# Performance work log

Hardware: AMD Instinct MI355X
Metric: run time of the kernel (lower is better)

Reference implementation:

```python
import jax, jax.numpy as jnp
import numpy as np

K_DELTA = 2.0
K_AN = 2.0
N_CLASSES = 32


def _masked_mean(x, mask):
    m = mask.astype(x.dtype)
    return jnp.sum(x * m) / jnp.maximum(jnp.sum(m), 1.0)


def setup_inputs() -> dict:
    key = jax.random.key(0)
    k1, k2 = jax.random.split(key)
    logits = jax.random.normal(k1, (384, 1024), dtype=jnp.float32)
    labels = jax.random.randint(k2, (384,), 0, N_CLASSES)
    return {"logits": logits, "labels": labels}


def reference(logits, labels):
    # Faithful jit-safe translation: torch.where / torch.unique produce
    # dynamic-shaped index lists; here we return the equivalent boolean
    # masks over the full triplet / pair space instead.
    N = labels.shape[0]
    x = jax.lax.stop_gradient(logits)  # logits.detach()
    x = x / jnp.linalg.norm(x, axis=1, keepdims=True)  # F.normalize p=2 dim=1
    mat = -(x @ x.T)  # negative cosine similarity, symmetric [N, N]

    sames = labels[:, None] == labels[None, :]
    diffs = ~sames
    sames = sames & ~jnp.eye(N, dtype=bool)  # fill_diagonal_(0)
    # triplet validity mask over (anchor, positive, negative)
    trip = sames[:, :, None] & diffs[:, None, :]  # [N, N, N]

    # delta[a, p, n] = an_dist - ap_dist
    delta = mat[:, None, :] - mat[:, :, None]  # [N, N, N]

    # --- calc_loss_an branch: unique (anchor, negative) pairs ---
    # a pair (a, n) appears in some triplet iff diffs[a, n] and anchor a has
    # at least one positive; unique_filter canonicalizes to (min, max).
    has_pos = jnp.any(sames, axis=1)  # [N]
    upper = jnp.triu(jnp.ones((N, N), dtype=bool), k=1)
    pair_mask = upper & diffs & (has_pos[:, None] | has_pos[None, :])
    an_mean = _masked_mean(mat, pair_mask)
    beta = 1.0 + (-an_mean - 1.0) / K_AN  # self.update(an_dist_unique, 'an')
    an_pairs = pair_mask & (-mat >= beta)

    # --- epsilon update + semi-hard triplet selection ---
    eps = jnp.clip(_masked_mean(delta, trip) / K_DELTA, 0.0, 0.5)
    cond = trip & (delta <= eps) & (delta > 0.0)  # semi-hard

    return cond, an_pairs, eps, beta
```

## Files before the change

kernel.cpp:

```cpp
#include <hip/hip_runtime.h>
#include <stdint.h>

#define N 384
#define D 1024
#define N2 (N * N)
static constexpr size_t N3 = (size_t)N * N2;

static constexpr size_t PART_OFF = 0;
static constexpr size_t MAT_OFF  = 2359296;
static constexpr size_t INVN_OFF = 3538944;
static constexpr size_t TN_OFF   = 3542016;
static constexpr size_t TC_OFF   = 3545088;
static constexpr size_t ANS_OFF  = 3548160;
static constexpr size_t ANC_OFF  = 3551232;
static constexpr size_t HP_OFF   = 3554304;
static constexpr size_t SC_OFF   = 3555840;

static constexpr int GEMM_BLOCKS = 288;
static constexpr int FILL_BLOCKS = 2048;
static constexpr size_t FILL_F4  = 14192640;

__global__ __launch_bounds__(256) void k_invnorm(const float* __restrict__ x,
                                                 double* __restrict__ invn) {
  int w = threadIdx.x >> 6, lane = threadIdx.x & 63;
  int a = blockIdx.x * 4 + w;
  const float4* row = (const float4*)(x + (size_t)a * D);
  double s = 0.0;
#pragma unroll
  for (int j = 0; j < 4; ++j) {
    float4 v = row[lane + 64 * j];
    double dx = v.x, dy = v.y, dz = v.z, dw = v.w;
    s += dx * dx + dy * dy + dz * dz + dw * dw;
  }
#pragma unroll
  for (int m = 32; m; m >>= 1) s += __shfl_xor(s, m, 64);
  if (lane == 0) invn[a] = 1.0 / sqrt(s);
}

__global__ __launch_bounds__(256) void k_mega(const float* __restrict__ x,
                                              const double* __restrict__ invn,
                                              double* __restrict__ part,
                                              float4* __restrict__ outv) {
  __shared__ double As[64][32];
  __shared__ double Bs[64][32];
  int b = blockIdx.x;
  int t = threadIdx.x;
  if (b >= GEMM_BLOCKS) {
    size_t i = (size_t)(b - GEMM_BLOCKS) * 256 + t;
    const size_t stride = (size_t)FILL_BLOCKS * 256;
    float4 z = make_float4(0.f, 0.f, 0.f, 0.f);
    for (; i < FILL_F4; i += stride) outv[i] = z;
    return;
  }
  int bz = b / 144, rem = b % 144;
  int m0 = (rem % 12) * 32, n0 = (rem / 12) * 32, k0 = bz * 512;
  int tm = t & 15, tn = t >> 4;
  double a00 = 0, a01 = 0, a10 = 0, a11 = 0;
  for (int kc = 0; kc < 8; ++kc) {
    int kbase = k0 + kc * 64;
#pragma unroll
    for (int h = 0; h < 2; ++h) {
      int f = t + h * 256;
      int m = f & 31, kq = f >> 5;
      float4 va = *(const float4*)(x + (size_t)(m0 + m) * D + kbase + kq * 4);
      As[kq * 4 + 0][m] = (double)va.x; As[kq * 4 + 1][m] = (double)va.y;
      As[kq * 4 + 2][m] = (double)va.z; As[kq * 4 + 3][m] = (double)va.w;
      float4 vb = *(const float4*)(x + (size_t)(n0 + m) * D + kbase + kq * 4);
      Bs[kq * 4 + 0][m] = (double)vb.x; Bs[kq * 4 + 1][m] = (double)vb.y;
      Bs[kq * 4 + 2][m] = (double)vb.z; Bs[kq * 4 + 3][m] = (double)vb.w;
    }
    __syncthreads();
#pragma unroll 8
    for (int k = 0; k < 64; ++k) {
      double ax = As[k][2 * tm], ay = As[k][2 * tm + 1];
      double bx = Bs[k][2 * tn], by = Bs[k][2 * tn + 1];
      a00 = fma(ax, bx, a00);
      a01 = fma(ax, by, a01);
      a10 = fma(ay, bx, a10);
      a11 = fma(ay, by, a11);
    }
    __syncthreads();
  }
  int r0 = m0 + 2 * tm, c0 = n0 + 2 * tn;
  double i0 = invn[r0], i1 = invn[r0 + 1], j0 = invn[c0], j1 = invn[c0 + 1];
  double* o = part + (size_t)bz * N2;
  o[(size_t)r0 * N + c0]           = a00 * (i0 * j0);
  o[(size_t)r0 * N + c0 + 1]       = a01 * (i0 * j1);
  o[(size_t)(r0 + 1) * N + c0]     = a10 * (i1 * j0);
  o[(size_t)(r0 + 1) * N + c0 + 1] = a11 * (i1 * j1);
}

__global__ __launch_bounds__(384) void k_stats(const double* __restrict__ part,
                                               const int* __restrict__ labels,
                                               double* __restrict__ mat,
                                               double* __restrict__ tn,
                                               double* __restrict__ tc,
                                               double* __restrict__ ans,
                                               double* __restrict__ anc,
                                               int* __restrict__ hp) {
  __shared__ int labs[N];
  __shared__ int hist[32];
  __shared__ double cw[6][6];
  int a = blockIdx.x, t = threadIdx.x;
  int w = t >> 6, lane = t & 63;
  if (t < 32) hist[t] = 0;
  labs[t] = labels[t];
  __syncthreads();
  atomicAdd(&hist[labs[t] & 31], 1);
  __syncthreads();
  int la = labs[a];
  double m = -(part[(size_t)a * N + t] + part[(size_t)N2 + (size_t)a * N + t]);
  mat[(size_t)a * N + t] = m;
  bool same = (labs[t] == la) && (t != a);
  bool diff = (labs[t] != la);
  bool hpa = hist[la] >= 2;
  bool hpt = hist[labs[t]] >= 2;
  bool anm = (t > a) && diff && (hpa || hpt);

  double q[6];
  q[0] = same ? m : 0.0;
  q[1] = same ? 1.0 : 0.0;
  q[2] = diff ? m : 0.0;
  q[3] = diff ? 1.0 : 0.0;
  q[4] = anm ? m : 0.0;
  q[5] = anm ? 1.0 : 0.0;
#pragma unroll
  for (int i = 0; i < 6; ++i) {
#pragma unroll
    for (int s = 32; s; s >>= 1) q[i] += __shfl_xor(q[i], s, 64);
  }
  if (lane == 0) {
#pragma unroll
    for (int i = 0; i < 6; ++i) cw[w][i] = q[i];
  }
  __syncthreads();
  if (t == 0) {
    double r[6];
#pragma unroll
    for (int i = 0; i < 6; ++i) {
      double s = 0.0;
      for (int ww = 0; ww < 6; ++ww) s += cw[ww][i];
      r[i] = s;
    }
    tn[a]  = r[2] * r[1] - r[0] * r[3];
    tc[a]  = r[1] * r[3];
    ans[a] = r[4];
    anc[a] = r[5];
    hp[a]  = hpa ? 1 : 0;
  }
}

__global__ __launch_bounds__(64) void k_final(const double* __restrict__ tn,
                                              const double* __restrict__ tc,
                                              const double* __restrict__ ans,
                                              const double* __restrict__ anc,
                                              double* __restrict__ sc,
                                              float* __restrict__ out_tail) {
  int t = threadIdx.x;
  double vtn = 0, vtc = 0, vas = 0, vac = 0;
#pragma unroll
  for (int j = 0; j < 6; ++j) {
    vtn += tn[t + 64 * j];
    vtc += tc[t + 64 * j];
    vas += ans[t + 64 * j];
    vac += anc[t + 64 * j];
  }
#pragma unroll
  for (int s = 32; s; s >>= 1) {
    vtn += __shfl_xor(vtn, s, 64);
    vtc += __shfl_xor(vtc, s, 64);
    vas += __shfl_xor(vas, s, 64);
    vac += __shfl_xor(vac, s, 64);
  }
  if (t == 0) {
    double an_mean = vas / fmax(vac, 1.0);
    double beta = 1.0 + ((-an_mean) - 1.0) / 2.0;
    double em = vtn / fmax(vtc, 1.0);
    double eps = em / 2.0;
    eps = eps < 0.0 ? 0.0 : (eps > 0.5 ? 0.5 : eps);
    sc[0] = eps;
    sc[1] = beta;
    out_tail[0] = (float)eps;
    out_tail[1] = (float)beta;
  }
}

__global__ __launch_bounds__(256) void k_sparse(const double* __restrict__ mat,
                                                const int* __restrict__ labels,
                                                const int* __restrict__ hp,
                                                const double* __restrict__ sc,
                                                float* __restrict__ out) {
  __shared__ int labs[N];
  __shared__ int hpL[N];
  __shared__ double matA[N];
  __shared__ int list[N];
  __shared__ int cnt;
  int a = blockIdx.x, t = threadIdx.x;
  for (int i = t; i < N; i += 256) {
    labs[i] = labels[i];
    hpL[i] = hp[i];
    matA[i] = mat[(size_t)a * N + i];
  }
  if (t == 0) cnt = 0;
  __syncthreads();
  int la = labs[a];
  for (int i = t; i < N; i += 256) {
    if (labs[i] == la && i != a) list[atomicAdd(&cnt, 1)] = i;
  }
  __syncthreads();
  double eps = sc[0], beta = sc[1];
  int hpa = hpL[a];
  if (t < 96) {
    int b0 = t * 4;
    float r[4];
#pragma unroll
    for (int j = 0; j < 4; ++j) {
      int b = b0 + j;
      bool pm = (a < b) && (labs[b] != la) && (hpa || hpL[b]);
      r[j] = (pm && (-matA[b] >= beta)) ? 1.0f : 0.0f;
    }
    *((float4*)(out + N3 + (size_t)a * N + b0)) = make_float4(r[0], r[1], r[2], r[3]);
  }
  int nc = cnt;
  for (int base = 0; base < nc; base += 2) {
    int rr = base + (t / 96);
    if (t < 192 && rr < nc) {
      int p = list[rr];
      double mp = matA[p];
      int n0 = (t % 96) * 4;
      float r[4];
#pragma unroll
      for (int j = 0; j < 4; ++j) {
        int n = n0 + j;
        double d = matA[n] - mp;
        r[j] = ((labs[n] != la) && (d > 0.0) && (d <= eps)) ? 1.0f : 0.0f;
      }
      *((float4*)(out + (size_t)a * N2 + (size_t)p * N + n0)) =
          make_float4(r[0], r[1], r[2], r[3]);
    }
  }
}

extern "C" void kernel_launch(void* const* d_in, const int* in_sizes, int n_in,
                              void* d_out, int out_size, void* d_ws, size_t ws_size,
                              hipStream_t stream) {
  const float* logits = (const float*)d_in[0];
  const int* labels = (const int*)d_in[1];
  float* out = (float*)d_out;
  char* ws = (char*)d_ws;
  double* part = (double*)(ws + PART_OFF);
  double* mat  = (double*)(ws + MAT_OFF);
  double* invn = (double*)(ws + INVN_OFF);
  double* tn   = (double*)(ws + TN_OFF);
  double* tc   = (double*)(ws + TC_OFF);
  double* ans  = (double*)(ws + ANS_OFF);
  double* anc  = (double*)(ws + ANC_OFF);
  int* hp      = (int*)(ws + HP_OFF);
  double* sc   = (double*)(ws + SC_OFF);

  k_invnorm<<<dim3(96), dim3(256), 0, stream>>>(logits, invn);
  k_mega<<<dim3(GEMM_BLOCKS + FILL_BLOCKS), dim3(256), 0, stream>>>(
      logits, invn, part, (float4*)out);
  k_stats<<<dim3(N), dim3(384), 0, stream>>>(part, labels, mat, tn, tc, ans,
                                             anc, hp);
  k_final<<<dim3(1), dim3(64), 0, stream>>>(tn, tc, ans, anc, sc,
                                            out + N3 + N2);
  k_sparse<<<dim3(N), dim3(256), 0, stream>>>(mat, labels, hp, sc, out);
}
```

Measured before the change: 59.19 us.

## Fuse norm into GEMM, drop split-K, skip redundant zero fill, inline final reduction

Removes the separate inverse-norm kernel by accumulating squared norms while staging GEMM tiles, and computes each block's norms from shared memory. Split-K is removed, so the GEMM writes negated mat directly and k_stats no longer sums two partials. The zero fill now skips (a,p) rows that k_sparse will overwrite anyway, which cuts write traffic but adds an integer division and a label lookup per float4. The final scalar reduction is recomputed by every k_sparse block, which removes a kernel launch at the cost of redundant tiny reductions. Dropping split-K halves the GEMM block count (144), which lowers parallelism in the GEMM part.

Measured after the change: 83.32 us. +40.8%, slower.

```diff
diff --git a/kernel.cpp b/kernel.cpp
--- a/kernel.cpp
+++ b/kernel.cpp
@@ -6,68 +6,64 @@
 #define N2 (N * N)
 static constexpr size_t N3 = (size_t)N * N2;
 
-static constexpr size_t PART_OFF = 0;
-static constexpr size_t MAT_OFF  = 2359296;
-static constexpr size_t INVN_OFF = 3538944;
-static constexpr size_t TN_OFF   = 3542016;
-static constexpr size_t TC_OFF   = 3545088;
-static constexpr size_t ANS_OFF  = 3548160;
-static constexpr size_t ANC_OFF  = 3551232;
-static constexpr size_t HP_OFF   = 3554304;
-static constexpr size_t SC_OFF   = 3555840;
-
-static constexpr int GEMM_BLOCKS = 288;
+static constexpr size_t MAT_OFF = 0;
+static constexpr size_t TN_OFF  = 1179648;
+static constexpr size_t TC_OFF  = 1182720;
+static constexpr size_t ANS_OFF = 1185792;
+static constexpr size_t ANC_OFF = 1188864;
+static constexpr size_t HP_OFF  = 1191936;
+
+static constexpr int GEMM_BLOCKS = 144;
 static constexpr int FILL_BLOCKS = 2048;
-static constexpr size_t FILL_F4  = 14192640;
-
-__global__ __launch_bounds__(256) void k_invnorm(const float* __restrict__ x,
-                                                 double* __restrict__ invn) {
-  int w = threadIdx.x >> 6, lane = threadIdx.x & 63;
-  int a = blockIdx.x * 4 + w;
-  const float4* row = (const float4*)(x + (size_t)a * D);
-  double s = 0.0;
-#pragma unroll
-  for (int j = 0; j < 4; ++j) {
-    float4 v = row[lane + 64 * j];
-    double dx = v.x, dy = v.y, dz = v.z, dw = v.w;
-    s += dx * dx + dy * dy + dz * dz + dw * dw;
-  }
-#pragma unroll
-  for (int m = 32; m; m >>= 1) s += __shfl_xor(s, m, 64);
-  if (lane == 0) invn[a] = 1.0 / sqrt(s);
-}
+static constexpr int COND_F4     = 14155776;
 
 __global__ __launch_bounds__(256) void k_mega(const float* __restrict__ x,
-                                              const double* __restrict__ invn,
-                                              double* __restrict__ part,
+                                              const int* __restrict__ labels,
+                                              double* __restrict__ mat,
                                               float4* __restrict__ outv) {
   __shared__ double As[64][32];
   __shared__ double Bs[64][32];
+  __shared__ double sqred[2][32][8];
+  __shared__ double invnA[32], invnB[32];
+  __shared__ int labsF[N];
   int b = blockIdx.x;
   int t = threadIdx.x;
+
   if (b >= GEMM_BLOCKS) {
-    size_t i = (size_t)(b - GEMM_BLOCKS) * 256 + t;
-    const size_t stride = (size_t)FILL_BLOCKS * 256;
-    float4 z = make_float4(0.f, 0.f, 0.f, 0.f);
-    for (; i < FILL_F4; i += stride) outv[i] = z;
+    for (int i = t; i < N; i += 256) labsF[i] = labels[i];
+    __syncthreads();
+    int i = (b - GEMM_BLOCKS) * 256 + t;
+    const int stride = FILL_BLOCKS * 256;
+    const float4 z = make_float4(0.f, 0.f, 0.f, 0.f);
+    for (; i < COND_F4; i += stride) {
+      int a = i / 36864;
+      int rem = i - a * 36864;
+      int p = rem / 96;
+      if (!(labsF[p] == labsF[a] && p != a)) outv[i] = z;
+    }
     return;
   }
-  int bz = b / 144, rem = b % 144;
-  int m0 = (rem % 12) * 32, n0 = (rem / 12) * 32, k0 = bz * 512;
+
+  int m0 = (b % 12) * 32, n0 = (b / 12) * 32;
   int tm = t & 15, tn = t >> 4;
   double a00 = 0, a01 = 0, a10 = 0, a11 = 0;
-  for (int kc = 0; kc < 8; ++kc) {
-    int kbase = k0 + kc * 64;
+  double sqA = 0, sqB = 0;
+  for (int kc = 0; kc < 16; ++kc) {
+    int kbase = kc * 64;
 #pragma unroll
     for (int h = 0; h < 2; ++h) {
       int f = t + h * 256;
       int m = f & 31, kq = f >> 5;
       float4 va = *(const float4*)(x + (size_t)(m0 + m) * D + kbase + kq * 4);
-      As[kq * 4 + 0][m] = (double)va.x; As[kq * 4 + 1][m] = (double)va.y;
-      As[kq * 4 + 2][m] = (double)va.z; As[kq * 4 + 3][m] = (double)va.w;
+      double ax = va.x, ay = va.y, az = va.z, aw = va.w;
+      As[kq * 4 + 0][m] = ax; As[kq * 4 + 1][m] = ay;
+      As[kq * 4 + 2][m] = az; As[kq * 4 + 3][m] = aw;
+      sqA += ax * ax + ay * ay + az * az + aw * aw;
       float4 vb = *(const float4*)(x + (size_t)(n0 + m) * D + kbase + kq * 4);
-      Bs[kq * 4 + 0][m] = (double)vb.x; Bs[kq * 4 + 1][m] = (double)vb.y;
-      Bs[kq * 4 + 2][m] = (double)vb.z; Bs[kq * 4 + 3][m] = (double)vb.w;
+      double bx = vb.x, by = vb.y, bz = vb.z, bw = vb.w;
+      Bs[kq * 4 + 0][m] = bx; Bs[kq * 4 + 1][m] = by;
+      Bs[kq * 4 + 2][m] = bz; Bs[kq * 4 + 3][m] = bw;
+      sqB += bx * bx + by * by + bz * bz + bw * bw;
     }
     __syncthreads();
 #pragma unroll 8
@@ -81,18 +77,29 @@
     }
     __syncthreads();
   }
+  sqred[0][t & 31][t >> 5] = sqA;
+  sqred[1][t & 31][t >> 5] = sqB;
+  __syncthreads();
+  if (t < 64) {
+    int which = t >> 5, m = t & 31;
+    double s = 0.0;
+#pragma unroll
+    for (int j = 0; j < 8; ++j) s += sqred[which][m][j];
+    double inv = 1.0 / sqrt(s);
+    if (which) invnB[m] = inv; else invnA[m] = inv;
+  }
+  __syncthreads();
   int r0 = m0 + 2 * tm, c0 = n0 + 2 * tn;
-  double i0 = invn[r0], i1 = invn[r0 + 1], j0 = invn[c0], j1 = invn[c0 + 1];
-  double* o = part + (size_t)bz * N2;
-  o[(size_t)r0 * N + c0]           = a00 * (i0 * j0);
-  o[(size_t)r0 * N + c0 + 1]       = a01 * (i0 * j1);
-  o[(size_t)(r0 + 1) * N + c0]     = a10 * (i1 * j0);
-  o[(size_t)(r0 + 1) * N + c0 + 1] = a11 * (i1 * j1);
-}
-
-__global__ __launch_bounds__(384) void k_stats(const double* __restrict__ part,
+  double i0 = invnA[2 * tm], i1 = invnA[2 * tm + 1];
+  double j0 = invnB[2 * tn], j1 = invnB[2 * tn + 1];
+  mat[(size_t)r0 * N + c0]           = -(a00 * (i0 * j0));
+  mat[(size_t)r0 * N + c0 + 1]       = -(a01 * (i0 * j1));
+  mat[(size_t)(r0 + 1) * N + c0]     = -(a10 * (i1 * j0));
+  mat[(size_t)(r0 + 1) * N + c0 + 1] = -(a11 * (i1 * j1));
+}
+
+__global__ __launch_bounds__(384) void k_stats(const double* __restrict__ mat,
                                                const int* __restrict__ labels,
-                                               double* __restrict__ mat,
                                                double* __restrict__ tn,
                                                double* __restrict__ tc,
                                                double* __restrict__ ans,
@@ -109,8 +116,7 @@
   atomicAdd(&hist[labs[t] & 31], 1);
   __syncthreads();
   int la = labs[a];
-  double m = -(part[(size_t)a * N + t] + part[(size_t)N2 + (size_t)a * N + t]);
-  mat[(size_t)a * N + t] = m;
+  double m = mat[(size_t)a * N + t];
   bool same = (labs[t] == la) && (t != a);
   bool diff = (labs[t] != la);
   bool hpa = hist[la] >= 2;
@@ -150,51 +156,20 @@
   }
 }
 
-__global__ __launch_bounds__(64) void k_final(const double* __restrict__ tn,
-                                              const double* __restrict__ tc,
-                                              const double* __restrict__ ans,
-                                              const double* __restrict__ anc,
-                                              double* __restrict__ sc,
-                                              float* __restrict__ out_tail) {
-  int t = threadIdx.x;
-  double vtn = 0, vtc = 0, vas = 0, vac = 0;
-#pragma unroll
-  for (int j = 0; j < 6; ++j) {
-    vtn += tn[t + 64 * j];
-    vtc += tc[t + 64 * j];
-    vas += ans[t + 64 * j];
-    vac += anc[t + 64 * j];
-  }
-#pragma unroll
-  for (int s = 32; s; s >>= 1) {
-    vtn += __shfl_xor(vtn, s, 64);
-    vtc += __shfl_xor(vtc, s, 64);
-    vas += __shfl_xor(vas, s, 64);
-    vac += __shfl_xor(vac, s, 64);
-  }
-  if (t == 0) {
-    double an_mean = vas / fmax(vac, 1.0);
-    double beta = 1.0 + ((-an_mean) - 1.0) / 2.0;
-    double em = vtn / fmax(vtc, 1.0);
-    double eps = em / 2.0;
-    eps = eps < 0.0 ? 0.0 : (eps > 0.5 ? 0.5 : eps);
-    sc[0] = eps;
-    sc[1] = beta;
-    out_tail[0] = (float)eps;
-    out_tail[1] = (float)beta;
-  }
-}
-
 __global__ __launch_bounds__(256) void k_sparse(const double* __restrict__ mat,
                                                 const int* __restrict__ labels,
                                                 const int* __restrict__ hp,
-                                                const double* __restrict__ sc,
+                                                const double* __restrict__ tn,
+                                                const double* __restrict__ tc,
+                                                const double* __restrict__ ans,
+                                                const double* __restrict__ anc,
                                                 float* __restrict__ out) {
   __shared__ int labs[N];
   __shared__ int hpL[N];
   __shared__ double matA[N];
   __shared__ int list[N];
   __shared__ int cnt;
+  __shared__ double sEps, sBeta;
   int a = blockIdx.x, t = threadIdx.x;
   for (int i = t; i < N; i += 256) {
     labs[i] = labels[i];
@@ -202,13 +177,41 @@
     matA[i] = mat[(size_t)a * N + i];
   }
   if (t == 0) cnt = 0;
+  if (t < 64) {
+    double vtn = 0, vtc = 0, vas = 0, vac = 0;
+#pragma unroll
+    for (int j = 0; j < 6; ++j) {
+      int idx = t + 64 * j;
+      vtn += tn[idx]; vtc += tc[idx]; vas += ans[idx]; vac += anc[idx];
+    }
+#pragma unroll
+    for (int s = 32; s; s >>= 1) {
+      vtn += __shfl_xor(vtn, s, 64);
+      vtc += __shfl_xor(vtc, s, 64);
+      vas += __shfl_xor(vas, s, 64);
+      vac += __shfl_xor(vac, s, 64);
+    }
+    if (t == 0) {
+      double an_mean = vas / fmax(vac, 1.0);
+      double beta = 1.0 + ((-an_mean) - 1.0) / 2.0;
+      double em = vtn / fmax(vtc, 1.0);
+      double eps = em / 2.0;
+      eps = eps < 0.0 ? 0.0 : (eps > 0.5 ? 0.5 : eps);
+      sEps = eps;
+      sBeta = beta;
+      if (a == 0) {
+        out[N3 + N2]     = (float)eps;
+        out[N3 + N2 + 1] = (float)beta;
+      }
+    }
+  }
   __syncthreads();
   int la = labs[a];
   for (int i = t; i < N; i += 256) {
     if (labs[i] == la && i != a) list[atomicAdd(&cnt, 1)] = i;
   }
   __syncthreads();
-  double eps = sc[0], beta = sc[1];
+  double eps = sEps, beta = sBeta;
   int hpa = hpL[a];
   if (t < 96) {
     int b0 = t * 4;
@@ -219,7 +222,8 @@
       bool pm = (a < b) && (labs[b] != la) && (hpa || hpL[b]);
       r[j] = (pm && (-matA[b] >= beta)) ? 1.0f : 0.0f;
     }
-    *((float4*)(out + N3 + (size_t)a * N + b0)) = make_float4(r[0], r[1], r[2], r[3]);
+    *((float4*)(out + N3 + (size_t)a * N + b0)) =
+        make_float4(r[0], r[1], r[2], r[3]);
   }
   int nc = cnt;
   for (int base = 0; base < nc; base += 2) {
@@ -248,22 +252,16 @@
   const int* labels = (const int*)d_in[1];
   float* out = (float*)d_out;
   char* ws = (char*)d_ws;
-  double* part = (double*)(ws + PART_OFF);
-  double* mat  = (double*)(ws + MAT_OFF);
-  double* invn = (double*)(ws + INVN_OFF);
-  double* tn   = (double*)(ws + TN_OFF);
-  double* tc   = (double*)(ws + TC_OFF);
-  double* ans  = (double*)(ws + ANS_OFF);
-  double* anc  = (double*)(ws + ANC_OFF);
-  int* hp      = (int*)(ws + HP_OFF);
-  double* sc   = (double*)(ws + SC_OFF);
-
-  k_invnorm<<<dim3(96), dim3(256), 0, stream>>>(logits, invn);
+  double* mat = (double*)(ws + MAT_OFF);
+  double* tn  = (double*)(ws + TN_OFF);
+  double* tc  = (double*)(ws + TC_OFF);
+  double* ans = (double*)(ws + ANS_OFF);
+  double* anc = (double*)(ws + ANC_OFF);
+  int* hp     = (int*)(ws + HP_OFF);
+
   k_mega<<<dim3(GEMM_BLOCKS + FILL_BLOCKS), dim3(256), 0, stream>>>(
-      logits, invn, part, (float4*)out);
-  k_stats<<<dim3(N), dim3(384), 0, stream>>>(part, labels, mat, tn, tc, ans,
-                                             anc, hp);
-  k_final<<<dim3(1), dim3(64), 0, stream>>>(tn, tc, ans, anc, sc,
-                                            out + N3 + N2);
-  k_sparse<<<dim3(N), dim3(256), 0, stream>>>(mat, labels, hp, sc, out);
-}
+      logits, labels, mat, (float4*)out);
+  k_stats<<<dim3(N), dim3(384), 0, stream>>>(mat, labels, tn, tc, ans, anc, hp);
+  k_sparse<<<dim3(N), dim3(256), 0, stream>>>(mat, labels, hp, tn, tc, ans,
+                                              anc, out);
+}
```

## Fold norm and final reduction kernels into neighbors, raise GEMM split-K to 4

Applied to the files above, without the earlier changes.

The row-norm computation moves into the fused GEMM+zero-fill launch as extra blocks. Normalization scaling moves from the GEMM epilogue into the stats kernel. The GEMM's split-K factor doubles to 4 slices for more parallel blocks, and the tiny single-block final reduction kernel is removed by having every sparse block recompute eps/beta redundantly. This cuts two launches and their serialization, in exchange for a larger partial-sum buffer, four reads per element in stats, and redundant reductions in each sparse block.

Result: faster. 52.47 us (-11.4%).

```diff
diff --git a/kernel.cpp b/kernel.cpp
--- a/kernel.cpp
+++ b/kernel.cpp
@@ -7,56 +7,57 @@
 static constexpr size_t N3 = (size_t)N * N2;
 
 static constexpr size_t PART_OFF = 0;
-static constexpr size_t MAT_OFF  = 2359296;
-static constexpr size_t INVN_OFF = 3538944;
-static constexpr size_t TN_OFF   = 3542016;
-static constexpr size_t TC_OFF   = 3545088;
-static constexpr size_t ANS_OFF  = 3548160;
-static constexpr size_t ANC_OFF  = 3551232;
-static constexpr size_t HP_OFF   = 3554304;
-static constexpr size_t SC_OFF   = 3555840;
-
-static constexpr int GEMM_BLOCKS = 288;
+static constexpr size_t MAT_OFF  = 4718592;
+static constexpr size_t INVN_OFF = 5898240;
+static constexpr size_t TN_OFF   = 5901312;
+static constexpr size_t TC_OFF   = 5904384;
+static constexpr size_t ANS_OFF  = 5907456;
+static constexpr size_t ANC_OFF  = 5910528;
+static constexpr size_t HP_OFF   = 5913600;
+
+static constexpr int GEMM_BLOCKS = 576;
+static constexpr int NORM_BLOCKS = 96;
 static constexpr int FILL_BLOCKS = 2048;
-static constexpr size_t FILL_F4  = 14192640;
-
-__global__ __launch_bounds__(256) void k_invnorm(const float* __restrict__ x,
-                                                 double* __restrict__ invn) {
-  int w = threadIdx.x >> 6, lane = threadIdx.x & 63;
-  int a = blockIdx.x * 4 + w;
-  const float4* row = (const float4*)(x + (size_t)a * D);
-  double s = 0.0;
-#pragma unroll
-  for (int j = 0; j < 4; ++j) {
-    float4 v = row[lane + 64 * j];
-    double dx = v.x, dy = v.y, dz = v.z, dw = v.w;
-    s += dx * dx + dy * dy + dz * dz + dw * dw;
-  }
-#pragma unroll
-  for (int m = 32; m; m >>= 1) s += __shfl_xor(s, m, 64);
-  if (lane == 0) invn[a] = 1.0 / sqrt(s);
-}
+static constexpr int FILL_F4     = 14192640;
 
 __global__ __launch_bounds__(256) void k_mega(const float* __restrict__ x,
-                                              const double* __restrict__ invn,
                                               double* __restrict__ part,
+                                              double* __restrict__ invn,
                                               float4* __restrict__ outv) {
   __shared__ double As[64][32];
   __shared__ double Bs[64][32];
   int b = blockIdx.x;
   int t = threadIdx.x;
-  if (b >= GEMM_BLOCKS) {
-    size_t i = (size_t)(b - GEMM_BLOCKS) * 256 + t;
-    const size_t stride = (size_t)FILL_BLOCKS * 256;
-    float4 z = make_float4(0.f, 0.f, 0.f, 0.f);
+
+  if (b >= GEMM_BLOCKS + NORM_BLOCKS) {
+    int i = (b - GEMM_BLOCKS - NORM_BLOCKS) * 256 + t;
+    const int stride = FILL_BLOCKS * 256;
+    const float4 z = make_float4(0.f, 0.f, 0.f, 0.f);
     for (; i < FILL_F4; i += stride) outv[i] = z;
     return;
   }
+  if (b >= GEMM_BLOCKS) {
+    int w = t >> 6, lane = t & 63;
+    int a = (b - GEMM_BLOCKS) * 4 + w;
+    const float4* row = (const float4*)(x + (size_t)a * D);
+    double s = 0.0;
+#pragma unroll
+    for (int j = 0; j < 4; ++j) {
+      float4 v = row[lane + 64 * j];
+      double dx = v.x, dy = v.y, dz = v.z, dw = v.w;
+      s += dx * dx + dy * dy + dz * dz + dw * dw;
+    }
+#pragma unroll
+    for (int m = 32; m; m >>= 1) s += __shfl_xor(s, m, 64);
+    if (lane == 0) invn[a] = 1.0 / sqrt(s);
+    return;
+  }
+
   int bz = b / 144, rem = b % 144;
-  int m0 = (rem % 12) * 32, n0 = (rem / 12) * 32, k0 = bz * 512;
+  int m0 = (rem % 12) * 32, n0 = (rem / 12) * 32, k0 = bz * 256;
   int tm = t & 15, tn = t >> 4;
   double a00 = 0, a01 = 0, a10 = 0, a11 = 0;
-  for (int kc = 0; kc < 8; ++kc) {
+  for (int kc = 0; kc < 4; ++kc) {
     int kbase = k0 + kc * 64;
 #pragma unroll
     for (int h = 0; h < 2; ++h) {
@@ -81,16 +82,16 @@
     }
     __syncthreads();
   }
+  double* o = part + (size_t)bz * N2;
   int r0 = m0 + 2 * tm, c0 = n0 + 2 * tn;
-  double i0 = invn[r0], i1 = invn[r0 + 1], j0 = invn[c0], j1 = invn[c0 + 1];
-  double* o = part + (size_t)bz * N2;
-  o[(size_t)r0 * N + c0]           = a00 * (i0 * j0);
-  o[(size_t)r0 * N + c0 + 1]       = a01 * (i0 * j1);
-  o[(size_t)(r0 + 1) * N + c0]     = a10 * (i1 * j0);
-  o[(size_t)(r0 + 1) * N + c0 + 1] = a11 * (i1 * j1);
+  o[(size_t)r0 * N + c0]           = a00;
+  o[(size_t)r0 * N + c0 + 1]       = a01;
+  o[(size_t)(r0 + 1) * N + c0]     = a10;
+  o[(size_t)(r0 + 1) * N + c0 + 1] = a11;
 }
 
 __global__ __launch_bounds__(384) void k_stats(const double* __restrict__ part,
+                                               const double* __restrict__ invn,
                                                const int* __restrict__ labels,
                                                double* __restrict__ mat,
                                                double* __restrict__ tn,
@@ -109,8 +110,13 @@
   atomicAdd(&hist[labs[t] & 31], 1);
   __syncthreads();
   int la = labs[a];
-  double m = -(part[(size_t)a * N + t] + part[(size_t)N2 + (size_t)a * N + t]);
-  mat[(size_t)a * N + t] = m;
+  size_t idx = (size_t)a * N + t;
+  double s = part[idx];
+  s += part[(size_t)N2 + idx];
+  s += part[2 * (size_t)N2 + idx];
+  s += part[3 * (size_t)N2 + idx];
+  double m = -(s * (invn[a] * invn[t]));
+  mat[idx] = m;
   bool same = (labs[t] == la) && (t != a);
   bool diff = (labs[t] != la);
   bool hpa = hist[la] >= 2;
@@ -127,7 +133,7 @@
 #pragma unroll
   for (int i = 0; i < 6; ++i) {
 #pragma unroll
-    for (int s = 32; s; s >>= 1) q[i] += __shfl_xor(q[i], s, 64);
+    for (int s2 = 32; s2; s2 >>= 1) q[i] += __shfl_xor(q[i], s2, 64);
   }
   if (lane == 0) {
 #pragma unroll
@@ -138,9 +144,9 @@
     double r[6];
 #pragma unroll
     for (int i = 0; i < 6; ++i) {
-      double s = 0.0;
-      for (int ww = 0; ww < 6; ++ww) s += cw[ww][i];
-      r[i] = s;
+      double s3 = 0.0;
+      for (int ww = 0; ww < 6; ++ww) s3 += cw[ww][i];
+      r[i] = s3;
     }
     tn[a]  = r[2] * r[1] - r[0] * r[3];
     tc[a]  = r[1] * r[3];
@@ -150,51 +156,20 @@
   }
 }
 
-__global__ __launch_bounds__(64) void k_final(const double* __restrict__ tn,
-                                              const double* __restrict__ tc,
-                                              const double* __restrict__ ans,
-                                              const double* __restrict__ anc,
-                                              double* __restrict__ sc,
-                                              float* __restrict__ out_tail) {
-  int t = threadIdx.x;
-  double vtn = 0, vtc = 0, vas = 0, vac = 0;
-#pragma unroll
-  for (int j = 0; j < 6; ++j) {
-    vtn += tn[t + 64 * j];
-    vtc += tc[t + 64 * j];
-    vas += ans[t + 64 * j];
-    vac += anc[t + 64 * j];
-  }
-#pragma unroll
-  for (int s = 32; s; s >>= 1) {
-    vtn += __shfl_xor(vtn, s, 64);
-    vtc += __shfl_xor(vtc, s, 64);
-    vas += __shfl_xor(vas, s, 64);
-    vac += __shfl_xor(vac, s, 64);
-  }
-  if (t == 0) {
-    double an_mean = vas / fmax(vac, 1.0);
-    double beta = 1.0 + ((-an_mean) - 1.0) / 2.0;
-    double em = vtn / fmax(vtc, 1.0);
-    double eps = em / 2.0;
-    eps = eps < 0.0 ? 0.0 : (eps > 0.5 ? 0.5 : eps);
-    sc[0] = eps;
-    sc[1] = beta;
-    out_tail[0] = (float)eps;
-    out_tail[1] = (float)beta;
-  }
-}
-
 __global__ __launch_bounds__(256) void k_sparse(const double* __restrict__ mat,
                                                 const int* __restrict__ labels,
                                                 const int* __restrict__ hp,
-                                                const double* __restrict__ sc,
+                                                const double* __restrict__ tn,
+                                                const double* __restrict__ tc,
+                                                const double* __restrict__ ans,
+                                                const double* __restrict__ anc,
                                                 float* __restrict__ out) {
   __shared__ int labs[N];
   __shared__ int hpL[N];
   __shared__ double matA[N];
   __shared__ int list[N];
   __shared__ int cnt;
+  __shared__ double sEps, sBeta;
   int a = blockIdx.x, t = threadIdx.x;
   for (int i = t; i < N; i += 256) {
     labs[i] = labels[i];
@@ -202,13 +177,41 @@
     matA[i] = mat[(size_t)a * N + i];
   }
   if (t == 0) cnt = 0;
+  if (t < 64) {
+    double vtn = 0, vtc = 0, vas = 0, vac = 0;
+#pragma unroll
+    for (int j = 0; j < 6; ++j) {
+      int idx = t + 64 * j;
+      vtn += tn[idx]; vtc += tc[idx]; vas += ans[idx]; vac += anc[idx];
+    }
+#pragma unroll
+    for (int s = 32; s; s >>= 1) {
+      vtn += __shfl_xor(vtn, s, 64);
+      vtc += __shfl_xor(vtc, s, 64);
+      vas += __shfl_xor(vas, s, 64);
+      vac += __shfl_xor(vac, s, 64);
+    }
+    if (t == 0) {
+      double an_mean = vas / fmax(vac, 1.0);
+      double beta = 1.0 + ((-an_mean) - 1.0) / 2.0;
+      double em = vtn / fmax(vtc, 1.0);
+      double eps = em / 2.0;
+      eps = eps < 0.0 ? 0.0 : (eps > 0.5 ? 0.5 : eps);
+      sEps = eps;
+      sBeta = beta;
+      if (a == 0) {
+        out[N3 + N2]     = (float)eps;
+        out[N3 + N2 + 1] = (float)beta;
+      }
+    }
+  }
   __syncthreads();
   int la = labs[a];
   for (int i = t; i < N; i += 256) {
     if (labs[i] == la && i != a) list[atomicAdd(&cnt, 1)] = i;
   }
   __syncthreads();
-  double eps = sc[0], beta = sc[1];
+  double eps = sEps, beta = sBeta;
   int hpa = hpL[a];
   if (t < 96) {
     int b0 = t * 4;
@@ -219,7 +222,8 @@
       bool pm = (a < b) && (labs[b] != la) && (hpa || hpL[b]);
       r[j] = (pm && (-matA[b] >= beta)) ? 1.0f : 0.0f;
     }
-    *((float4*)(out + N3 + (size_t)a * N + b0)) = make_float4(r[0], r[1], r[2], r[3]);
+    *((float4*)(out + N3 + (size_t)a * N + b0)) =
+        make_float4(r[0], r[1], r[2], r[3]);
   }
   int nc = cnt;
   for (int base = 0; base < nc; base += 2) {
@@ -256,14 +260,11 @@
   double* ans  = (double*)(ws + ANS_OFF);
   double* anc  = (double*)(ws + ANC_OFF);
   int* hp      = (int*)(ws + HP_OFF);
-  double* sc   = (double*)(ws + SC_OFF);
-
-  k_invnorm<<<dim3(96), dim3(256), 0, stream>>>(logits, invn);
-  k_mega<<<dim3(GEMM_BLOCKS + FILL_BLOCKS), dim3(256), 0, stream>>>(
-      logits, invn, part, (float4*)out);
-  k_stats<<<dim3(N), dim3(384), 0, stream>>>(part, labels, mat, tn, tc, ans,
-                                             anc, hp);
-  k_final<<<dim3(1), dim3(64), 0, stream>>>(tn, tc, ans, anc, sc,
-                                            out + N3 + N2);
-  k_sparse<<<dim3(N), dim3(256), 0, stream>>>(mat, labels, hp, sc, out);
-}
+
+  k_mega<<<dim3(GEMM_BLOCKS + NORM_BLOCKS + FILL_BLOCKS), dim3(256), 0,
+           stream>>>(logits, part, invn, (float4*)out);
+  k_stats<<<dim3(N), dim3(384), 0, stream>>>(part, invn, labels, mat, tn, tc,
+                                             ans, anc, hp);
+  k_sparse<<<dim3(N), dim3(256), 0, stream>>>(mat, labels, hp, tn, tc, ans,
+                                              anc, out);
+}
```
